# Performance work log

Hardware: AMD Instinct MI355X
Metric: run time of the kernel (lower is better)

Reference implementation:

```python
import jax, jax.numpy as jnp
import numpy as np

B, H, L, DK = 8, 8, 512, 64
LK, C = 512, 5


def setup_inputs() -> dict:
    key = jax.random.key(0)
    ks = jax.random.split(key, 6)
    d_in = LK * H * DK  # l_k * d_model
    return {
        "Q": jax.random.normal(ks[0], (B, H, L, DK), dtype=jnp.float32),
        "K": jax.random.normal(ks[1], (B, H, LK, DK), dtype=jnp.float32),
        # scale by 1/sqrt(fan_in) so softmax inputs are sane
        "W_proj": jax.random.normal(ks[2], (d_in, C), dtype=jnp.float32) / np.sqrt(d_in),
        "b_proj": jnp.zeros((C,), dtype=jnp.float32),
        "W_q": jax.random.normal(ks[3], (C, C), dtype=jnp.float32) / np.sqrt(C),
        "b_q": jnp.zeros((C,), dtype=jnp.float32),
        "W_k": jax.random.normal(ks[4], (C, C), dtype=jnp.float32) / np.sqrt(C),
        "b_k": jnp.zeros((C,), dtype=jnp.float32),
    }


def reference(Q, K, W_proj, b_proj, W_q, b_q, W_k, b_k):
    b, h, l, d_k = Q.shape
    l_k = K.shape[2]
    n_clusters = b_proj.shape[0]
    hd = h * d_k

    # cluster projections over flattened K
    ck_proj = K.reshape(b, -1) @ W_proj + b_proj            # (b, C)
    cluster_q = jax.nn.softmax(ck_proj @ W_q + b_q, axis=-1)  # (b, C)
    cluster_k = jax.nn.softmax(ck_proj @ W_k + b_k, axis=-1)  # (b, C)

    # Gaussian likelihood term (torch.std is unbiased -> ddof=1)
    mu = jnp.mean(cluster_q, axis=0)                         # (C,)
    sigma = jax.nn.softplus(jnp.std(cluster_k, axis=0, ddof=1))
    log_prob = (-0.5 * ((cluster_k - mu) / sigma) ** 2
                - jnp.log(sigma) - 0.5 * jnp.log(2.0 * jnp.pi))
    # CrossEntropyLoss with prob targets: mean_b(-sum target*log_softmax(input))
    ce = jnp.mean(-jnp.sum(cluster_q * jax.nn.log_softmax(cluster_q, axis=-1), axis=-1))
    loss = -jnp.mean(log_prob) + ce

    # cluster assignment per batch element
    inds = jnp.argmax(cluster_q, axis=-1)                    # (b,) in [0, C)

    # The original per-cluster loop with where(K_cluster != i+1, K_inds, 0) then
    # mean(dim=0)[0] reduces to: mean over batch of K_re[:,0,:] masked where
    # assignment != i+1, broadcast across l_k.
    K_re = K.reshape(b, l_k, hd)
    row0 = K_re[:, 0, :]                                     # (b, hd)
    keep = (inds[None, :] != (jnp.arange(n_clusters) + 1)[:, None]).astype(Q.dtype)  # (C, b)
    means = (keep @ row0) / b                                # (C, hd)

    # broadcast to (b, C, l_k, hd) then raw reshape to (b, h, C, l_k, d_k)
    cm = jnp.broadcast_to(means[None, :, None, :], (b, n_clusters, l_k, hd))
    cm = cm.reshape(b, h, n_clusters, l_k, d_k)

    scale = 1.0 / np.sqrt(d_k)
    scores_qk = jnp.einsum('bhqd,bhkd->bhqk', Q, K) * scale          # (b,h,l,l_k)
    scores_qc = jnp.einsum('bhqd,bhckd->bhcqk', Q, cm) * scale       # (b,h,C,l,l_k)
    # max over cat([qk, qc], dim=2) == elementwise max of qk and max_c qc
    final_score = jnp.maximum(scores_qk, jnp.max(scores_qc, axis=2))
    return final_score, loss
```

## Files before the change

### kernel.cpp

```cpp
#include <hip/hip_runtime.h>
#include <math.h>

#define NB 8
#define NH 8
#define SEQ 512
#define DK 64
#define NC 5
#define D_IN 262144
#define OUT_SCORE (NB*NH*SEQ*SEQ)

typedef short short8 __attribute__((ext_vector_type(8)));
typedef float f32x16 __attribute__((ext_vector_type(16)));

__device__ __forceinline__ short f2bf(float f) {
  unsigned u = __float_as_uint(f);
  u += 0x7fffu + ((u >> 16) & 1u);
  return (short)(u >> 16);
}
__device__ __forceinline__ short8 pack8(float4 a, float4 b) {
  short8 r;
  r[0] = f2bf(a.x); r[1] = f2bf(a.y); r[2] = f2bf(a.z); r[3] = f2bf(a.w);
  r[4] = f2bf(b.x); r[5] = f2bf(b.y); r[6] = f2bf(b.z); r[7] = f2bf(b.w);
  return r;
}

__global__ __launch_bounds__(256) void proj_kernel(const float* __restrict__ K,
                                                   const float* __restrict__ Wp,
                                                   float* __restrict__ ck) {
  int i4 = blockIdx.x * 256 + threadIdx.x;
  const float4* Wp4 = (const float4*)Wp;
  float w[20];
#pragma unroll
  for (int t = 0; t < 5; ++t) {
    float4 v = Wp4[i4 * 5 + t];
    w[4*t+0] = v.x; w[4*t+1] = v.y; w[4*t+2] = v.z; w[4*t+3] = v.w;
  }
  float acc[NB][NC];
#pragma unroll
  for (int b = 0; b < NB; ++b)
#pragma unroll
    for (int c = 0; c < NC; ++c) acc[b][c] = 0.f;
#pragma unroll
  for (int b = 0; b < NB; ++b) {
    float4 kv = ((const float4*)(K + (size_t)b * D_IN))[i4];
    float ke[4] = {kv.x, kv.y, kv.z, kv.w};
#pragma unroll
    for (int e = 0; e < 4; ++e)
#pragma unroll
      for (int c = 0; c < NC; ++c)
        acc[b][c] = fmaf(ke[e], w[5*e + c], acc[b][c]);
  }

  __shared__ float red[4][NB * NC];
  int wave = threadIdx.x >> 6;
  int lane = threadIdx.x & 63;
#pragma unroll
  for (int bc = 0; bc < NB * NC; ++bc) {
    float v = acc[bc / NC][bc % NC];
#pragma unroll
    for (int off = 32; off > 0; off >>= 1) v += __shfl_down(v, off);
    if (lane == 0) red[wave][bc] = v;
  }
  __syncthreads();
  if (threadIdx.x < NB * NC) {
    float s = red[0][threadIdx.x] + red[1][threadIdx.x] +
              red[2][threadIdx.x] + red[3][threadIdx.x];
    atomicAdd(&ck[threadIdx.x], s);
  }
}

__global__ __launch_bounds__(256) void small_kernel(
    const float* __restrict__ K, const float* __restrict__ ck_raw,
    const float* __restrict__ bp, const float* __restrict__ Wq,
    const float* __restrict__ bq, const float* __restrict__ Wk,
    const float* __restrict__ bk, float* __restrict__ means,
    float* __restrict__ loss_out) {
  __shared__ float cq[NB][NC], ckk[NB][NC], ce_sh[NB];
  __shared__ int inds[NB];
  int t = threadIdx.x;
  if (t < NB) {
    float cp[NC], zq[NC], zk[NC];
#pragma unroll
    for (int c = 0; c < NC; ++c) cp[c] = ck_raw[t * NC + c] + bp[c];
#pragma unroll
    for (int c = 0; c < NC; ++c) { zq[c] = bq[c]; zk[c] = bk[c]; }
#pragma unroll
    for (int j = 0; j < NC; ++j)
#pragma unroll
      for (int c = 0; c < NC; ++c) {
        zq[c] = fmaf(cp[j], Wq[j * NC + c], zq[c]);
        zk[c] = fmaf(cp[j], Wk[j * NC + c], zk[c]);
      }
    float m = zq[0];
#pragma unroll
    for (int c = 1; c < NC; ++c) m = fmaxf(m, zq[c]);
    float e[NC], s = 0.f;
#pragma unroll
    for (int c = 0; c < NC; ++c) { e[c] = expf(zq[c] - m); s += e[c]; }
    float inv = 1.f / s;
    float p[NC];
#pragma unroll
    for (int c = 0; c < NC; ++c) { p[c] = e[c] * inv; cq[t][c] = p[c]; }
    int am = 0; float bv = p[0];
#pragma unroll
    for (int c = 1; c < NC; ++c) if (p[c] > bv) { bv = p[c]; am = c; }
    inds[t] = am;
    float se = 0.f;
#pragma unroll
    for (int c = 0; c < NC; ++c) se += expf(p[c] - bv);
    float lse = bv + logf(se);
    float ceb = 0.f;
#pragma unroll
    for (int c = 0; c < NC; ++c) ceb -= p[c] * (p[c] - lse);
    ce_sh[t] = ceb;
    m = zk[0];
#pragma unroll
    for (int c = 1; c < NC; ++c) m = fmaxf(m, zk[c]);
    s = 0.f;
#pragma unroll
    for (int c = 0; c < NC; ++c) { e[c] = expf(zk[c] - m); s += e[c]; }
    inv = 1.f / s;
#pragma unroll
    for (int c = 0; c < NC; ++c) ckk[t][c] = e[c] * inv;
  }
  __syncthreads();
  if (t == 0) {
    float mu[NC];
#pragma unroll
    for (int c = 0; c < NC; ++c) {
      float sm = 0.f;
      for (int b = 0; b < NB; ++b) sm += cq[b][c];
      mu[c] = sm * 0.125f;
    }
    float loss_lp = 0.f;
#pragma unroll
    for (int c = 0; c < NC; ++c) {
      float sm = 0.f;
      for (int b = 0; b < NB; ++b) sm += ckk[b][c];
      float mk = sm * 0.125f;
      float var = 0.f;
      for (int b = 0; b < NB; ++b) {
        float d = ckk[b][c] - mk;
        var += d * d;
      }
      var *= (1.f / 7.f);
      float sd = sqrtf(var);
      float sigma = log1pf(expf(sd));
      float ls = logf(sigma);
      for (int b = 0; b < NB; ++b) {
        float z = (ckk[b][c] - mu[c]) / sigma;
        loss_lp += -0.5f * z * z - ls - 0.91893853320467274f;
      }
    }
    float ce = 0.f;
    for (int b = 0; b < NB; ++b) ce += ce_sh[b];
    ce *= 0.125f;
    loss_out[0] = -(loss_lp / 40.f) + ce;
  }
  __syncthreads();
  for (int idx = t; idx < NC * 512; idx += 256) {
    int c = idx >> 9, j = idx & 511;
    float sm = 0.f;
#pragma unroll
    for (int b = 0; b < NB; ++b)
      if (inds[b] != c + 1) sm += K[(size_t)b * D_IN + j];
    means[idx] = sm * 0.125f;
  }
}

__global__ __launch_bounds__(256) void score_kernel(const float* __restrict__ Q,
                                                    const float* __restrict__ K,
                                                    const float* __restrict__ means,
                                                    float* __restrict__ out) {
  const int bh = blockIdx.x;
  const int h  = bh & 7;
  const int qblk = blockIdx.y << 7;
  const int kblk = blockIdx.z << 7;
  const int tid = threadIdx.x;
  const int w = tid >> 6, lane = tid & 63;
  const int lo5 = lane & 31, hi = lane >> 5;
  const int wq = ((w >> 1) << 6), wk = ((w & 1) << 6);

  const float* Qb = Q + (size_t)bh * (SEQ * DK);
  const float* Kb = K + (size_t)bh * (SEQ * DK);

  short8 afrag[2][4];
#pragma unroll
  for (int i = 0; i < 2; ++i)
#pragma unroll
    for (int s = 0; s < 4; ++s) {
      const float* p = Qb + (size_t)(qblk + wq + i * 32 + lo5) * DK + s * 16 + hi * 8;
      afrag[i][s] = pack8(*(const float4*)p, *(const float4*)(p + 4));
    }

  f32x16 zero;
#pragma unroll
  for (int x = 0; x < 16; ++x) zero[x] = 0.f;

  const int cmin = (5 * h) >> 3;
  const int cmax = (5 * h + 4) >> 3;
  const int r = lo5 & 7;
  const int csel = (lo5 & 8) ? cmax : cmin;
  f32x16 aq0 = zero, aq1 = zero;
#pragma unroll
  for (int s = 0; s < 4; ++s) {
    const float* mp = means + csel * 512 + r * 64 + s * 16 + hi * 8;
    short8 bm = pack8(*(const float4*)mp, *(const float4*)(mp + 4));
    aq0 = __builtin_amdgcn_mfma_f32_32x32x16_bf16(afrag[0][s], bm, aq0, 0, 0, 0);
    aq1 = __builtin_amdgcn_mfma_f32_32x32x16_bf16(afrag[1][s], bm, aq1, 0, 0, 0);
  }
  float qcv[2][16];
  const int sb = lane & 32;
#pragma unroll
  for (int reg = 0; reg < 16; ++reg) {
    float v0 = aq0[reg], v1 = aq1[reg];
    float a0 = __shfl(v0, sb + r),     a1 = __shfl(v1, sb + r);
    float b0 = __shfl(v0, sb + 8 + r), b1 = __shfl(v1, sb + 8 + r);
    qcv[0][reg] = fmaxf(a0, b0) * 0.125f;
    qcv[1][reg] = fmaxf(a1, b1) * 0.125f;
  }

  f32x16 acc00 = zero, acc01 = zero, acc10 = zero, acc11 = zero;
#pragma unroll
  for (int s = 0; s < 4; ++s) {
    const float* p0 = Kb + (size_t)(kblk + wk + lo5) * DK + s * 16 + hi * 8;
    const float* p1 = Kb + (size_t)(kblk + wk + 32 + lo5) * DK + s * 16 + hi * 8;
    short8 bf0 = pack8(*(const float4*)p0, *(const float4*)(p0 + 4));
    short8 bf1 = pack8(*(const float4*)p1, *(const float4*)(p1 + 4));
    acc00 = __builtin_amdgcn_mfma_f32_32x32x16_bf16(afrag[0][s], bf0, acc00, 0, 0, 0);
    acc01 = __builtin_amdgcn_mfma_f32_32x32x16_bf16(afrag[0][s], bf1, acc01, 0, 0, 0);
    acc10 = __builtin_amdgcn_mfma_f32_32x32x16_bf16(afrag[1][s], bf0, acc10, 0, 0, 0);
    acc11 = __builtin_amdgcn_mfma_f32_32x32x16_bf16(afrag[1][s], bf1, acc11, 0, 0, 0);
  }

  float* ob = out + (size_t)bh * (SEQ * SEQ);
  const int col0 = kblk + wk + lo5;
#pragma unroll
  for (int reg = 0; reg < 16; ++reg) {
    int rowbase = qblk + wq + (reg & 3) + ((reg >> 2) << 3) + (hi << 2);
    float q0 = qcv[0][reg], q1 = qcv[1][reg];
    ob[(size_t)(rowbase)      * SEQ + col0]      = fmaxf(acc00[reg] * 0.125f, q0);
    ob[(size_t)(rowbase)      * SEQ + col0 + 32] = fmaxf(acc01[reg] * 0.125f, q0);
    ob[(size_t)(rowbase + 32) * SEQ + col0]      = fmaxf(acc10[reg] * 0.125f, q1);
    ob[(size_t)(rowbase + 32) * SEQ + col0 + 32] = fmaxf(acc11[reg] * 0.125f, q1);
  }
}

extern "C" void kernel_launch(void* const* d_in, const int* in_sizes, int n_in,
                              void* d_out, int out_size, void* d_ws, size_t ws_size,
                              hipStream_t stream) {
  const float* Q  = (const float*)d_in[0];
  const float* K  = (const float*)d_in[1];
  const float* Wp = (const float*)d_in[2];
  const float* bp = (const float*)d_in[3];
  const float* Wq = (const float*)d_in[4];
  const float* bq = (const float*)d_in[5];
  const float* Wk = (const float*)d_in[6];
  const float* bk = (const float*)d_in[7];
  float* out = (float*)d_out;

  float* ck = (float*)d_ws;
  float* means = ck + 64;

  hipMemsetAsync(ck, 0, NB * NC * sizeof(float), stream);
  proj_kernel<<<256, 256, 0, stream>>>(K, Wp, ck);
  small_kernel<<<1, 256, 0, stream>>>(K, ck, bp, Wq, bq, Wk, bk, means,
                                      out + OUT_SCORE);
  dim3 grid(64, 4, 4);
  score_kernel<<<grid, 256, 0, stream>>>(Q, K, means, out);
}
```

Measured before the change: 147.2 us.

## Stage bf16 Q/K tiles in LDS and swap MFMA operands for float4 stores

Each block now loads its 128x64 Q and K tiles cooperatively, converts them to bf16 once and stores them in padded shared memory. Before, each wave converted its own fragments straight from global memory. The MFMA operands are swapped so every lane holds one query row with 16 key values. This lets the epilogue write float4 vectors instead of scalar stores, and the cluster-score max no longer needs lane shuffles. It adds a shared-memory buffer and a barrier, and each store instruction now covers shorter contiguous runs per row.

```diff
diff --git a/kernel.cpp b/kernel.cpp
--- a/kernel.cpp
+++ b/kernel.cpp
@@ -168,10 +168,14 @@
   }
 }
 
+#define LDSTRIDE 72
 __global__ __launch_bounds__(256) void score_kernel(const float* __restrict__ Q,
                                                     const float* __restrict__ K,
                                                     const float* __restrict__ means,
                                                     float* __restrict__ out) {
+  __shared__ short Qs[128 * LDSTRIDE];
+  __shared__ short Ks[128 * LDSTRIDE];
+
   const int bh = blockIdx.x;
   const int h  = bh & 7;
   const int qblk = blockIdx.y << 7;
@@ -179,70 +183,94 @@
   const int tid = threadIdx.x;
   const int w = tid >> 6, lane = tid & 63;
   const int lo5 = lane & 31, hi = lane >> 5;
-  const int wq = ((w >> 1) << 6), wk = ((w & 1) << 6);
-
-  const float* Qb = Q + (size_t)bh * (SEQ * DK);
-  const float* Kb = K + (size_t)bh * (SEQ * DK);
-
-  short8 afrag[2][4];
-#pragma unroll
-  for (int i = 0; i < 2; ++i)
-#pragma unroll
-    for (int s = 0; s < 4; ++s) {
-      const float* p = Qb + (size_t)(qblk + wq + i * 32 + lo5) * DK + s * 16 + hi * 8;
-      afrag[i][s] = pack8(*(const float4*)p, *(const float4*)(p + 4));
-    }
-
-  f32x16 zero;
-#pragma unroll
-  for (int x = 0; x < 16; ++x) zero[x] = 0.f;
+  const int wq = (w >> 1) << 6;
+  const int wk = (w & 1) << 6;
+
+  const float* Qg = Q + (size_t)bh * (SEQ * DK) + (size_t)qblk * DK;
+  const float* Kg = K + (size_t)bh * (SEQ * DK) + (size_t)kblk * DK;
+
+#pragma unroll
+  for (int i = 0; i < 4; ++i) {
+    int f8 = i * 256 + tid;
+    int row = f8 >> 3, c8 = f8 & 7;
+    const float4* qp = (const float4*)(Qg + row * DK + c8 * 8);
+    const float4* kp = (const float4*)(Kg + row * DK + c8 * 8);
+    *(short8*)&Qs[row * LDSTRIDE + c8 * 8] = pack8(qp[0], qp[1]);
+    *(short8*)&Ks[row * LDSTRIDE + c8 * 8] = pack8(kp[0], kp[1]);
+  }
 
   const int cmin = (5 * h) >> 3;
   const int cmax = (5 * h + 4) >> 3;
-  const int r = lo5 & 7;
-  const int csel = (lo5 & 8) ? cmax : cmin;
+  short8 mfrag[4];
+#pragma unroll
+  for (int s = 0; s < 4; ++s) {
+    float4 a = {0.f, 0.f, 0.f, 0.f}, b = {0.f, 0.f, 0.f, 0.f};
+    if (lo5 < 16) {
+      int c = (lo5 < 8) ? cmin : cmax;
+      const float* mp = means + c * 512 + (lo5 & 7) * 64 + s * 16 + hi * 8;
+      a = *(const float4*)mp;
+      b = *(const float4*)(mp + 4);
+    }
+    mfrag[s] = pack8(a, b);
+  }
+
+  __syncthreads();
+
+  f32x16 zero;
+#pragma unroll
+  for (int x = 0; x < 16; ++x) zero[x] = 0.f;
+
+  const int fcol = hi * 16 + 0;
+
   f32x16 aq0 = zero, aq1 = zero;
 #pragma unroll
   for (int s = 0; s < 4; ++s) {
-    const float* mp = means + csel * 512 + r * 64 + s * 16 + hi * 8;
-    short8 bm = pack8(*(const float4*)mp, *(const float4*)(mp + 4));
-    aq0 = __builtin_amdgcn_mfma_f32_32x32x16_bf16(afrag[0][s], bm, aq0, 0, 0, 0);
-    aq1 = __builtin_amdgcn_mfma_f32_32x32x16_bf16(afrag[1][s], bm, aq1, 0, 0, 0);
-  }
-  float qcv[2][16];
-  const int sb = lane & 32;
-#pragma unroll
-  for (int reg = 0; reg < 16; ++reg) {
-    float v0 = aq0[reg], v1 = aq1[reg];
-    float a0 = __shfl(v0, sb + r),     a1 = __shfl(v1, sb + r);
-    float b0 = __shfl(v0, sb + 8 + r), b1 = __shfl(v1, sb + 8 + r);
-    qcv[0][reg] = fmaxf(a0, b0) * 0.125f;
-    qcv[1][reg] = fmaxf(a1, b1) * 0.125f;
+    short8 b0 = *(const short8*)&Qs[(wq + lo5)      * LDSTRIDE + s * 16 + hi * 8];
+    short8 b1 = *(const short8*)&Qs[(wq + 32 + lo5) * LDSTRIDE + s * 16 + hi * 8];
+    aq0 = __builtin_amdgcn_mfma_f32_32x32x16_bf16(mfrag[s], b0, aq0, 0, 0, 0);
+    aq1 = __builtin_amdgcn_mfma_f32_32x32x16_bf16(mfrag[s], b1, aq1, 0, 0, 0);
+  }
+  float qcv[2][4];
+#pragma unroll
+  for (int e = 0; e < 4; ++e) {
+    qcv[0][e] = fmaxf(aq0[e], aq0[4 + e]) * 0.125f;
+    qcv[1][e] = fmaxf(aq1[e], aq1[4 + e]) * 0.125f;
   }
 
   f32x16 acc00 = zero, acc01 = zero, acc10 = zero, acc11 = zero;
 #pragma unroll
   for (int s = 0; s < 4; ++s) {
-    const float* p0 = Kb + (size_t)(kblk + wk + lo5) * DK + s * 16 + hi * 8;
-    const float* p1 = Kb + (size_t)(kblk + wk + 32 + lo5) * DK + s * 16 + hi * 8;
-    short8 bf0 = pack8(*(const float4*)p0, *(const float4*)(p0 + 4));
-    short8 bf1 = pack8(*(const float4*)p1, *(const float4*)(p1 + 4));
-    acc00 = __builtin_amdgcn_mfma_f32_32x32x16_bf16(afrag[0][s], bf0, acc00, 0, 0, 0);
-    acc01 = __builtin_amdgcn_mfma_f32_32x32x16_bf16(afrag[0][s], bf1, acc01, 0, 0, 0);
-    acc10 = __builtin_amdgcn_mfma_f32_32x32x16_bf16(afrag[1][s], bf0, acc10, 0, 0, 0);
-    acc11 = __builtin_amdgcn_mfma_f32_32x32x16_bf16(afrag[1][s], bf1, acc11, 0, 0, 0);
+    int co = s * 16 + hi * 8;
+    short8 a0 = *(const short8*)&Ks[(wk + lo5)      * LDSTRIDE + co];
+    short8 a1 = *(const short8*)&Ks[(wk + 32 + lo5) * LDSTRIDE + co];
+    short8 b0 = *(const short8*)&Qs[(wq + lo5)      * LDSTRIDE + co];
+    short8 b1 = *(const short8*)&Qs[(wq + 32 + lo5) * LDSTRIDE + co];
+    acc00 = __builtin_amdgcn_mfma_f32_32x32x16_bf16(a0, b0, acc00, 0, 0, 0);
+    acc01 = __builtin_amdgcn_mfma_f32_32x32x16_bf16(a0, b1, acc01, 0, 0, 0);
+    acc10 = __builtin_amdgcn_mfma_f32_32x32x16_bf16(a1, b0, acc10, 0, 0, 0);
+    acc11 = __builtin_amdgcn_mfma_f32_32x32x16_bf16(a1, b1, acc11, 0, 0, 0);
   }
 
   float* ob = out + (size_t)bh * (SEQ * SEQ);
-  const int col0 = kblk + wk + lo5;
-#pragma unroll
-  for (int reg = 0; reg < 16; ++reg) {
-    int rowbase = qblk + wq + (reg & 3) + ((reg >> 2) << 3) + (hi << 2);
-    float q0 = qcv[0][reg], q1 = qcv[1][reg];
-    ob[(size_t)(rowbase)      * SEQ + col0]      = fmaxf(acc00[reg] * 0.125f, q0);
-    ob[(size_t)(rowbase)      * SEQ + col0 + 32] = fmaxf(acc01[reg] * 0.125f, q0);
-    ob[(size_t)(rowbase + 32) * SEQ + col0]      = fmaxf(acc10[reg] * 0.125f, q1);
-    ob[(size_t)(rowbase + 32) * SEQ + col0 + 32] = fmaxf(acc11[reg] * 0.125f, q1);
+  const int q0 = qblk + wq + lo5;
+  const int q1 = q0 + 32;
+  const int kb0 = kblk + wk + 4 * hi;
+#pragma unroll
+  for (int g = 0; g < 4; ++g) {
+    float4 o00, o01, o10, o11;
+    float* p00 = (float*)&o00; float* p01 = (float*)&o01;
+    float* p10 = (float*)&o10; float* p11 = (float*)&o11;
+#pragma unroll
+    for (int e = 0; e < 4; ++e) {
+      p00[e] = fmaxf(acc00[4 * g + e] * 0.125f, qcv[0][e]);
+      p01[e] = fmaxf(acc01[4 * g + e] * 0.125f, qcv[1][e]);
+      p10[e] = fmaxf(acc10[4 * g + e] * 0.125f, qcv[0][e]);
+      p11[e] = fmaxf(acc11[4 * g + e] * 0.125f, qcv[1][e]);
+    }
+    *(float4*)(ob + (size_t)q0 * SEQ + kb0 + 8 * g)      = o00;
+    *(float4*)(ob + (size_t)q1 * SEQ + kb0 + 8 * g)      = o01;
+    *(float4*)(ob + (size_t)q0 * SEQ + kb0 + 32 + 8 * g) = o10;
+    *(float4*)(ob + (size_t)q1 * SEQ + kb0 + 32 + 8 * g) = o11;
   }
 }
 
```

Result: no change. 148.2 us (+0.7%).
